# Optimization experiments

Hardware: AMD Instinct MI355X
Metric: run time of the kernel (lower is better)

## Reference

```python
import jax, jax.numpy as jnp
import numpy as np

KERNEL = (3, 3)
STRIDE = (1, 1)
DILATION = (1, 1)
PADDING = ((1, 1), (1, 1))


def setup_inputs() -> dict:
    key = jax.random.key(0)
    k1, k2 = jax.random.split(key)
    x = jax.random.normal(k1, (4096, 4096), dtype=jnp.float32)
    weight = jax.random.normal(k2, (9,), dtype=jnp.float32)
    bias = jnp.zeros((1,), dtype=jnp.float32)
    return {"x": x, "weight": weight, "bias": bias}


def reference(x, weight, bias):
    # convNdFunc: stride_transpose=1 -> repeat_interleave is identity;
    # pad(x, padding=1, 'constant', 0); view -> sliding 3x3 windows with
    # stride 1, dilation 1 over ALL dims of x; flatten window positions;
    # func = linear: flatten(3x3) @ weight + bias -> scalar per window;
    # reshape back to (H_out, W_out).
    # im2col via patches: [1, 9, H, W] (kernel taps stacked on channel axis)
    patches = jax.lax.conv_general_dilated_patches(
        x[None, None, :, :], KERNEL, STRIDE, list(PADDING),
        rhs_dilation=DILATION)
    out = jnp.einsum('kij,k->ij', patches[0], weight) + bias[0]
    return out
```

## Files before the change

### kernel.cpp

```cpp
#include <hip/hip_runtime.h>


#define H 4096
#define W 4096
#define COLS_PER_THREAD 4
#define ROWS_PER_THREAD 4
#define BLOCK 256

__global__ __launch_bounds__(BLOCK) void conv3x3_kernel(
    const float* __restrict__ x, const float* __restrict__ w9,
    const float* __restrict__ bias, float* __restrict__ out) {
    const int c = (blockIdx.x * BLOCK + threadIdx.x) * COLS_PER_THREAD;
    const int r0 = blockIdx.y * ROWS_PER_THREAD;
    if (c >= W || r0 >= H) return;

    float wv[9];
#pragma unroll
    for (int i = 0; i < 9; ++i) wv[i] = w9[i];
    const float b = bias[0];

    float4 v[6];
    float lf[6], rt[6];
#pragma unroll
    for (int i = 0; i < 6; ++i) {
        const int rr = r0 + i - 1;
        if (rr >= 0 && rr < H) {
            const float* row = x + (size_t)rr * W + c;
            v[i] = *(const float4*)row;
            lf[i] = (c > 0) ? row[-1] : 0.0f;
            rt[i] = (c + 4 < W) ? row[4] : 0.0f;
        } else {
            v[i] = make_float4(0.f, 0.f, 0.f, 0.f);
            lf[i] = 0.0f;
            rt[i] = 0.0f;
        }
    }

    float4 acc[4];
#pragma unroll
    for (int j = 0; j < 4; ++j) acc[j] = make_float4(b, b, b, b);

#pragma unroll
    for (int j = 0; j < 4; ++j) {
#pragma unroll
        for (int dr = 0; dr < 3; ++dr) {
            const int i = j + dr;
            const float w0 = wv[dr * 3 + 0];
            const float w1 = wv[dr * 3 + 1];
            const float w2 = wv[dr * 3 + 2];
            acc[j].x = fmaf(w0, lf[i],  fmaf(w1, v[i].x, fmaf(w2, v[i].y, acc[j].x)));
            acc[j].y = fmaf(w0, v[i].x, fmaf(w1, v[i].y, fmaf(w2, v[i].z, acc[j].y)));
            acc[j].z = fmaf(w0, v[i].y, fmaf(w1, v[i].z, fmaf(w2, v[i].w, acc[j].z)));
            acc[j].w = fmaf(w0, v[i].z, fmaf(w1, v[i].w, fmaf(w2, rt[i],  acc[j].w)));
        }
    }

#pragma unroll
    for (int j = 0; j < 4; ++j) {
        *(float4*)(out + (size_t)(r0 + j) * W + c) = acc[j];
    }
}

extern "C" void kernel_launch(void* const* d_in, const int* in_sizes, int n_in,
                              void* d_out, int out_size, void* d_ws, size_t ws_size,
                              hipStream_t stream) {
    const float* x = (const float*)d_in[0];
    const float* w = (const float*)d_in[1];
    const float* bias = (const float*)d_in[2];
    float* out = (float*)d_out;

    dim3 block(BLOCK, 1, 1);
    dim3 grid(W / (BLOCK * COLS_PER_THREAD), H / ROWS_PER_THREAD, 1);
    conv3x3_kernel<<<grid, block, 0, stream>>>(x, w, bias, out);
}
```

Before: 121.7 us.

## Stream rows through registers with prefetch and nontemporal output stores

Each thread now walks a 16-row vertical stripe in four steps instead of handling a single 4-row tile. The two halo rows are carried over in registers, which cuts redundant input reads from 6/4 to roughly 18/16 per output row. The next four rows are loaded before the current step's FMAs so memory latency overlaps compute. Output is written with nontemporal stores to avoid cache pollution, at the cost of higher register pressure and four times fewer blocks.

```diff
diff --git a/kernel.cpp b/kernel.cpp
--- a/kernel.cpp
+++ b/kernel.cpp
@@ -3,61 +3,101 @@
 
 #define H 4096
 #define W 4096
-#define COLS_PER_THREAD 4
-#define ROWS_PER_THREAD 4
+#define CPT 4
+#define RPT 4
+#define STEPS 4
 #define BLOCK 256
 
-__global__ __launch_bounds__(BLOCK) void conv3x3_kernel(
+typedef float vfloat4 __attribute__((ext_vector_type(4)));
+
+__global__ __launch_bounds__(BLOCK) void conv3x3_stripe(
     const float* __restrict__ x, const float* __restrict__ w9,
     const float* __restrict__ bias, float* __restrict__ out) {
-    const int c = (blockIdx.x * BLOCK + threadIdx.x) * COLS_PER_THREAD;
-    const int r0 = blockIdx.y * ROWS_PER_THREAD;
-    if (c >= W || r0 >= H) return;
+    const int c = (blockIdx.x * BLOCK + threadIdx.x) * CPT;
+    const int rbase = blockIdx.y * (STEPS * RPT);
 
     float wv[9];
 #pragma unroll
     for (int i = 0; i < 9; ++i) wv[i] = w9[i];
     const float b = bias[0];
 
-    float4 v[6];
+    vfloat4 v[6];
     float lf[6], rt[6];
+
 #pragma unroll
     for (int i = 0; i < 6; ++i) {
-        const int rr = r0 + i - 1;
+        const int rr = rbase - 1 + i;
         if (rr >= 0 && rr < H) {
             const float* row = x + (size_t)rr * W + c;
-            v[i] = *(const float4*)row;
+            v[i] = *(const vfloat4*)row;
             lf[i] = (c > 0) ? row[-1] : 0.0f;
-            rt[i] = (c + 4 < W) ? row[4] : 0.0f;
+            rt[i] = (c + CPT < W) ? row[CPT] : 0.0f;
         } else {
-            v[i] = make_float4(0.f, 0.f, 0.f, 0.f);
-            lf[i] = 0.0f;
-            rt[i] = 0.0f;
-        }
-    }
-
-    float4 acc[4];
-#pragma unroll
-    for (int j = 0; j < 4; ++j) acc[j] = make_float4(b, b, b, b);
-
-#pragma unroll
-    for (int j = 0; j < 4; ++j) {
-#pragma unroll
-        for (int dr = 0; dr < 3; ++dr) {
-            const int i = j + dr;
-            const float w0 = wv[dr * 3 + 0];
-            const float w1 = wv[dr * 3 + 1];
-            const float w2 = wv[dr * 3 + 2];
-            acc[j].x = fmaf(w0, lf[i],  fmaf(w1, v[i].x, fmaf(w2, v[i].y, acc[j].x)));
-            acc[j].y = fmaf(w0, v[i].x, fmaf(w1, v[i].y, fmaf(w2, v[i].z, acc[j].y)));
-            acc[j].z = fmaf(w0, v[i].y, fmaf(w1, v[i].z, fmaf(w2, v[i].w, acc[j].z)));
-            acc[j].w = fmaf(w0, v[i].z, fmaf(w1, v[i].w, fmaf(w2, rt[i],  acc[j].w)));
+            v[i] = (vfloat4)(0.f);
+            lf[i] = 0.f;
+            rt[i] = 0.f;
         }
     }
 
 #pragma unroll
-    for (int j = 0; j < 4; ++j) {
-        *(float4*)(out + (size_t)(r0 + j) * W + c) = acc[j];
+    for (int s = 0; s < STEPS; ++s) {
+        const int r0 = rbase + s * RPT;
+
+        vfloat4 nv[4];
+        float nlf[4], nrt[4];
+        if (s < STEPS - 1) {
+#pragma unroll
+            for (int k = 0; k < 4; ++k) {
+                const int rr = r0 + 5 + k;
+                if (rr < H) {
+                    const float* row = x + (size_t)rr * W + c;
+                    nv[k] = *(const vfloat4*)row;
+                    nlf[k] = (c > 0) ? row[-1] : 0.0f;
+                    nrt[k] = (c + CPT < W) ? row[CPT] : 0.0f;
+                } else {
+                    nv[k] = (vfloat4)(0.f);
+                    nlf[k] = 0.f;
+                    nrt[k] = 0.f;
+                }
+            }
+        }
+
+        vfloat4 acc[RPT];
+#pragma unroll
+        for (int j = 0; j < RPT; ++j) acc[j] = (vfloat4)(b);
+
+#pragma unroll
+        for (int j = 0; j < RPT; ++j) {
+#pragma unroll
+            for (int dr = 0; dr < 3; ++dr) {
+                const int i = j + dr;
+                const float w0 = wv[dr * 3 + 0];
+                const float w1 = wv[dr * 3 + 1];
+                const float w2 = wv[dr * 3 + 2];
+                acc[j].x = fmaf(w0, lf[i],  fmaf(w1, v[i].x, fmaf(w2, v[i].y, acc[j].x)));
+                acc[j].y = fmaf(w0, v[i].x, fmaf(w1, v[i].y, fmaf(w2, v[i].z, acc[j].y)));
+                acc[j].z = fmaf(w0, v[i].y, fmaf(w1, v[i].z, fmaf(w2, v[i].w, acc[j].z)));
+                acc[j].w = fmaf(w0, v[i].z, fmaf(w1, v[i].w, fmaf(w2, rt[i],  acc[j].w)));
+            }
+        }
+
+#pragma unroll
+        for (int j = 0; j < RPT; ++j) {
+            __builtin_nontemporal_store(acc[j],
+                (vfloat4*)(out + (size_t)(r0 + j) * W + c));
+        }
+
+        if (s < STEPS - 1) {
+            v[0] = v[4];  v[1] = v[5];
+            lf[0] = lf[4]; lf[1] = lf[5];
+            rt[0] = rt[4]; rt[1] = rt[5];
+#pragma unroll
+            for (int k = 0; k < 4; ++k) {
+                v[2 + k] = nv[k];
+                lf[2 + k] = nlf[k];
+                rt[2 + k] = nrt[k];
+            }
+        }
     }
 }
 
@@ -70,6 +110,6 @@
     float* out = (float*)d_out;
 
     dim3 block(BLOCK, 1, 1);
-    dim3 grid(W / (BLOCK * COLS_PER_THREAD), H / ROWS_PER_THREAD, 1);
-    conv3x3_kernel<<<grid, block, 0, stream>>>(x, w, bias, out);
+    dim3 grid(W / (BLOCK * CPT), H / (STEPS * RPT), 1);
+    conv3x3_stripe<<<grid, block, 0, stream>>>(x, w, bias, out);
 }
```

Result: faster. 113.8 us (-6.5%).
